# Optimization experiments

Hardware: AMD Instinct MI355X
Metric: run time of the kernel (lower is better)

The kernel has to match this reference:

```python
import jax, jax.numpy as jnp
import numpy as np

NUM_EMBEDDINGS = 1024
EMBEDDING_DIM = 256
COMMITMENT_COST = 0.25


def setup_inputs() -> dict:
    key = jax.random.key(0)
    k1, k2 = jax.random.split(key)
    x = jax.random.normal(k1, (32, EMBEDDING_DIM, 32, 32), dtype=jnp.float32)
    codebook = jax.random.uniform(
        k2, (NUM_EMBEDDINGS, EMBEDDING_DIM), dtype=jnp.float32,
        minval=-1.0 / NUM_EMBEDDINGS, maxval=1.0 / NUM_EMBEDDINGS)
    return {"x": x, "codebook": codebook}


def reference(x, codebook):
    # x: [B, C, H, W] -> [B, H, W, C]
    inputs = jnp.transpose(x, (0, 2, 3, 1))
    B, H, W, D = inputs.shape
    K = codebook.shape[0]
    flat = inputs.reshape(-1, D)  # [N, D]

    # squared L2 distances to each code: [N, K]
    distances = (jnp.sum(flat ** 2, axis=1, keepdims=True)
                 + jnp.sum(codebook ** 2, axis=1)
                 - 2.0 * flat @ codebook.T)
    idx = jnp.argmin(distances, axis=1)  # [N]

    # gather codes (equivalent to one-hot @ codebook, without materializing one-hot)
    quantized = codebook[idx].reshape(inputs.shape)

    e_latent_loss = jnp.mean((jax.lax.stop_gradient(quantized) - inputs) ** 2)
    q_latent_loss = jnp.mean((quantized - jax.lax.stop_gradient(inputs)) ** 2)
    loss = q_latent_loss + COMMITMENT_COST * e_latent_loss

    # straight-through estimator
    quantized_st = inputs + jax.lax.stop_gradient(quantized - inputs)

    # perplexity from code usage histogram (mean of one-hot encodings)
    N = flat.shape[0]
    avg_probs = jnp.zeros((K,), dtype=flat.dtype).at[idx].add(1.0) / N
    perplexity = jnp.exp(-jnp.sum(avg_probs * jnp.log(avg_probs + 1e-10)))

    out = jnp.transpose(quantized_st, (0, 3, 1, 2))  # back to [B, C, H, W]
    return (out, loss, perplexity)
```

## Files before the change

kernel.cpp:

```cpp
#include <hip/hip_runtime.h>
#include <hip/hip_fp16.h>

typedef _Float16 half8 __attribute__((ext_vector_type(8)));
typedef _Float16 half4v __attribute__((ext_vector_type(4)));
typedef __attribute__((ext_vector_type(4))) float f32x4;

#define OUT_ELEMS 8388608


__global__ __launch_bounds__(256) void prep_kernel(const float* __restrict__ cb,
        unsigned short* __restrict__ chs, float* __restrict__ sq,
        int* __restrict__ counts, float* __restrict__ loss) {
    const int t = threadIdx.x;
    if (blockIdx.x == 0) {
        ((int4*)counts)[t] = make_int4(0, 0, 0, 0);
        if (t == 0) *loss = 0.f;
    }
    const int row = blockIdx.x * 16 + (t >> 4);
    const int d0 = (t & 15) * 16;
    const float* src = cb + row * 256 + d0;
    half8 h0, h1;
    float s = 0.f;
#pragma unroll
    for (int i = 0; i < 16; ++i) {
        const float v = src[i];
        s += v * v;
        const _Float16 h = (_Float16)(v * 1024.f);
        if (i < 8) h0[i] = h; else h1[i - 8] = h;
    }
    *(half8*)(chs + row * 256 + d0)     = h0;
    *(half8*)(chs + row * 256 + d0 + 8) = h1;
#pragma unroll
    for (int off = 1; off < 16; off <<= 1) s += __shfl_xor(s, off);
    if ((t & 15) == 0) sq[row] = s;
}

__global__ __launch_bounds__(512, 2) void vq_kernel(
    const float* __restrict__ x, const float* __restrict__ cb,
    const unsigned short* __restrict__ chs, const float* __restrict__ sq,
    int* __restrict__ counts, float* __restrict__ loss_accum,
    float* __restrict__ out)
{
    __shared__ __align__(16) unsigned char Arena[65536];
    __shared__ float mv[4][128];
    __shared__ int   mk[4][128];
    __shared__ float xsqL[128];
    __shared__ int   codeL[128];
    __shared__ float wsum[2];

    const int t = threadIdx.x;
    const int lane = t & 63;
    const int w  = t >> 6;
    const int wg = w >> 1;
    const int wl = w & 1;
    const int m = lane & 15;
    const int q = lane >> 4;
    const int kb = wg << 8;
    const int rowb = wl << 6;
    const int bid = blockIdx.x;
    const int batch = bid >> 3;
    const int hwb = (bid & 7) << 7;

    unsigned short* XL = (unsigned short*)Arena;
    {
        const float* xg = x + (size_t)batch * 262144 + hwb;
#pragma unroll
        for (int p = 0; p < 4; ++p) {
            const int id = p * 512 + t;
            const int c4 = id >> 5;
            const int hw4 = id & 31;
            const float* s0 = xg + (size_t)(c4 * 4) * 1024 + hw4 * 4;
            const f32x4 v0 = *(const f32x4*)(s0);
            const f32x4 v1 = *(const f32x4*)(s0 + 1024);
            const f32x4 v2 = *(const f32x4*)(s0 + 2048);
            const f32x4 v3 = *(const f32x4*)(s0 + 3072);
#pragma unroll
            for (int j = 0; j < 4; ++j) {
                const int hw = hw4 * 4 + j;
                const int e = (((hw & 7) ^ ((hw >> 3) & 7)) << 1);
                half4v hv;
                hv[0] = (_Float16)v0[j];
                hv[1] = (_Float16)v1[j];
                hv[2] = (_Float16)v2[j];
                hv[3] = (_Float16)v3[j];
                *(half4v*)(XL + hw * 256 + ((c4 ^ e) << 2)) = hv;
            }
        }
    }
    __syncthreads();

    half8 Ah[4][8];
#pragma unroll
    for (int f = 0; f < 4; ++f) {
        const int hw = rowb + f * 16 + m;
        const unsigned short* row = XL + hw * 256;
        const int e = (((hw & 7) ^ ((hw >> 3) & 7)) << 1);
        float xs = 0.f;
#pragma unroll
        for (int ks = 0; ks < 8; ++ks) {
            const half8 a = *(const half8*)(row + (((8 * ks + 2 * q) ^ e) << 2));
            Ah[f][ks] = a;
#pragma unroll
            for (int j = 0; j < 8; ++j) { const float fv = (float)a[j]; xs = fmaf(fv, fv, xs); }
        }
        xs += __shfl_xor(xs, 16);
        xs += __shfl_xor(xs, 32);
        if (wg == 0 && q == 0) xsqL[hw] = xs;
    }

    float bestv[4][4];
    int   bestk[4][4];
#pragma unroll
    for (int f = 0; f < 4; ++f)
#pragma unroll
        for (int r = 0; r < 4; ++r) { bestv[f][r] = 3.4e38f; bestk[f][r] = 0; }

    float sc2 = sq[kb + m];

    const unsigned short* bgl = chs + (size_t)(kb + m) * 256 + q * 8;

    for (int s = 0; s < 16; ++s) {
        float sqn = 0.f;
        if (s + 1 < 16) sqn = sq[kb + (s + 1) * 16 + m];
        half8 Bf[8];
        const unsigned short* bp = bgl + s * 4096;
#pragma unroll
        for (int ks = 0; ks < 8; ++ks)
            Bf[ks] = *(const half8*)(bp + ks * 32);
        f32x4 a0 = {0.f,0.f,0.f,0.f}, a1 = {0.f,0.f,0.f,0.f};
        f32x4 a2 = {0.f,0.f,0.f,0.f}, a3 = {0.f,0.f,0.f,0.f};
#pragma unroll
        for (int ks = 0; ks < 8; ++ks) {
            a0 = __builtin_amdgcn_mfma_f32_16x16x32_f16(Ah[0][ks], Bf[ks], a0, 0, 0, 0);
            a1 = __builtin_amdgcn_mfma_f32_16x16x32_f16(Ah[1][ks], Bf[ks], a1, 0, 0, 0);
            a2 = __builtin_amdgcn_mfma_f32_16x16x32_f16(Ah[2][ks], Bf[ks], a2, 0, 0, 0);
            a3 = __builtin_amdgcn_mfma_f32_16x16x32_f16(Ah[3][ks], Bf[ks], a3, 0, 0, 0);
        }
        const int code = kb + s * 16 + m;
#pragma unroll
        for (int f = 0; f < 4; ++f) {
            const f32x4 a = (f == 0) ? a0 : (f == 1) ? a1 : (f == 2) ? a2 : a3;
#pragma unroll
            for (int r = 0; r < 4; ++r) {
                const float d0v = fmaf(-0.001953125f, a[r], sc2);
                if (d0v < bestv[f][r]) { bestv[f][r] = d0v; bestk[f][r] = code; }
            }
        }
        sc2 = sqn;
    }

#pragma unroll
    for (int f = 0; f < 4; ++f)
#pragma unroll
        for (int r = 0; r < 4; ++r) {
            float v = bestv[f][r];
            int   k = bestk[f][r];
#pragma unroll
            for (int d = 1; d < 16; d <<= 1) {
                const float ov = __shfl_xor(v, d);
                const int   ok = __shfl_xor(k, d);
                if (ov < v || (ov == v && ok < k)) { v = ov; k = ok; }
            }
            if (m == 0) {
                const int row = rowb + f * 16 + q * 4 + r;
                mv[wg][row] = v;
                mk[wg][row] = k;
            }
        }
    __syncthreads();

    if (t < 128) {
        float v = mv[0][t]; int k = mk[0][t];
#pragma unroll
        for (int g2 = 1; g2 < 4; ++g2) {
            const float vg = mv[g2][t];
            const int   kg = mk[g2][t];
            if (vg < v) { v = vg; k = kg; }
        }
        codeL[t] = k;
        atomicAdd(&counts[k], 1);
        float lp = xsqL[t] + v;
#pragma unroll
        for (int off = 32; off > 0; off >>= 1) lp += __shfl_down(lp, off);
        if ((t & 63) == 0) wsum[t >> 6] = lp;
    }
    __syncthreads();
    if (t == 0) atomicAdd(loss_accum, wsum[0] + wsum[1]);

    float* Q = (float*)Arena;
#pragma unroll
    for (int h = 0; h < 4; ++h) {
        {
            const int r = t & 31, seg = t >> 5;
            const float* src = cb + (size_t)codeL[h * 32 + r] * 256 + seg * 16;
#pragma unroll
            for (int i = 0; i < 4; ++i)
                *(f32x4*)&Q[r * 257 + seg * 16 + i * 4] = *(const f32x4*)(src + i * 4);
        }
        __syncthreads();
        {
            const int hw4 = (t & 7) * 4;
            const int c0 = t >> 3;
            float* dst = out + (size_t)batch * 262144 + hwb + h * 32 + hw4;
#pragma unroll
            for (int i = 0; i < 4; ++i) {
                const int c = c0 + i * 64;
                f32x4 v;
                v[0] = Q[(hw4 + 0) * 257 + c];
                v[1] = Q[(hw4 + 1) * 257 + c];
                v[2] = Q[(hw4 + 2) * 257 + c];
                v[3] = Q[(hw4 + 3) * 257 + c];
                *(f32x4*)(dst + (size_t)c * 1024) = v;
            }
        }
        if (h < 3) __syncthreads();
    }
}

__global__ __launch_bounds__(256) void finalize_kernel(
    const int* __restrict__ counts, const float* __restrict__ loss_accum,
    float* __restrict__ out)
{
    __shared__ float wsum[4];
    const int t = threadIdx.x;
    float s = 0.f;
#pragma unroll
    for (int mm = 0; mm < 4; ++mm) {
        const float p = (float)counts[t + 256 * mm] * (1.f / 32768.f);
        s += p * logf(p + 1e-10f);
    }
#pragma unroll
    for (int off = 32; off > 0; off >>= 1) s += __shfl_down(s, off);
    if ((t & 63) == 0) wsum[t >> 6] = s;
    __syncthreads();
    if (t == 0) {
        out[OUT_ELEMS]     = loss_accum[0] * (1.25f / 8388608.f);
        out[OUT_ELEMS + 1] = expf(-(wsum[0] + wsum[1] + wsum[2] + wsum[3]));
    }
}

extern "C" void kernel_launch(void* const* d_in, const int* in_sizes, int n_in,
                              void* d_out, int out_size, void* d_ws, size_t ws_size,
                              hipStream_t stream) {
    const float* x  = (const float*)d_in[0];
    const float* cb = (const float*)d_in[1];
    float* out = (float*)d_out;
    char* wsb = (char*)d_ws;
    int*            counts = (int*)(wsb + 0);
    float*          loss   = (float*)(wsb + 4096);
    float*          sq     = (float*)(wsb + 8192);
    unsigned short* chs    = (unsigned short*)(wsb + 16384);

    prep_kernel<<<64, 256, 0, stream>>>(cb, chs, sq, counts, loss);
    vq_kernel<<<256, 512, 0, stream>>>(x, cb, chs, sq, counts, loss, out);
    finalize_kernel<<<1, 256, 0, stream>>>(counts, loss, out);
}
```

Before: 134.7 us.

## Halve rows per block, pre-swizzle codebook fragments, pack best indices, nontemporal IO

```diff
diff --git a/kernel.cpp b/kernel.cpp
--- a/kernel.cpp
+++ b/kernel.cpp
@@ -28,25 +28,28 @@
         const _Float16 h = (_Float16)(v * 1024.f);
         if (i < 8) h0[i] = h; else h1[i - 8] = h;
     }
-    *(half8*)(chs + row * 256 + d0)     = h0;
-    *(half8*)(chs + row * 256 + d0 + 8) = h1;
+    const int g = row >> 8, st = (row >> 4) & 15, m = row & 15;
+    const int j0 = (t & 15) * 2;
+    const int ks = j0 >> 2, qq = j0 & 3;
+    unsigned short* dst = chs + (size_t)((((g * 16 + st) * 8 + ks) * 64) + m * 4 + qq) * 8;
+    *(half8*)dst       = h0;
+    *(half8*)(dst + 8) = h1;
 #pragma unroll
     for (int off = 1; off < 16; off <<= 1) s += __shfl_xor(s, off);
     if ((t & 15) == 0) sq[row] = s;
 }
 
-__global__ __launch_bounds__(512, 2) void vq_kernel(
+__global__ __launch_bounds__(512, 4) void vq_kernel(
     const float* __restrict__ x, const float* __restrict__ cb,
     const unsigned short* __restrict__ chs, const float* __restrict__ sq,
     int* __restrict__ counts, float* __restrict__ loss_accum,
     float* __restrict__ out)
 {
-    __shared__ __align__(16) unsigned char Arena[65536];
-    __shared__ float mv[4][128];
-    __shared__ int   mk[4][128];
-    __shared__ float xsqL[128];
-    __shared__ int   codeL[128];
-    __shared__ float wsum[2];
+    __shared__ __align__(16) unsigned char Arena[33024];
+    __shared__ float mv[4][64];
+    __shared__ int   mk[4][64];
+    __shared__ float xsqL[64];
+    __shared__ int   codeL[64];
 
     const int t = threadIdx.x;
     const int lane = t & 63;
@@ -56,24 +59,24 @@
     const int m = lane & 15;
     const int q = lane >> 4;
     const int kb = wg << 8;
-    const int rowb = wl << 6;
+    const int rowb = wl << 5;
     const int bid = blockIdx.x;
-    const int batch = bid >> 3;
-    const int hwb = (bid & 7) << 7;
+    const int batch = bid >> 4;
+    const int hwb = (bid & 15) << 6;
 
     unsigned short* XL = (unsigned short*)Arena;
     {
         const float* xg = x + (size_t)batch * 262144 + hwb;
 #pragma unroll
-        for (int p = 0; p < 4; ++p) {
+        for (int p = 0; p < 2; ++p) {
             const int id = p * 512 + t;
-            const int c4 = id >> 5;
-            const int hw4 = id & 31;
+            const int c4 = id >> 4;
+            const int hw4 = id & 15;
             const float* s0 = xg + (size_t)(c4 * 4) * 1024 + hw4 * 4;
-            const f32x4 v0 = *(const f32x4*)(s0);
-            const f32x4 v1 = *(const f32x4*)(s0 + 1024);
-            const f32x4 v2 = *(const f32x4*)(s0 + 2048);
-            const f32x4 v3 = *(const f32x4*)(s0 + 3072);
+            const f32x4 v0 = __builtin_nontemporal_load((const f32x4*)(s0));
+            const f32x4 v1 = __builtin_nontemporal_load((const f32x4*)(s0 + 1024));
+            const f32x4 v2 = __builtin_nontemporal_load((const f32x4*)(s0 + 2048));
+            const f32x4 v3 = __builtin_nontemporal_load((const f32x4*)(s0 + 3072));
 #pragma unroll
             for (int j = 0; j < 4; ++j) {
                 const int hw = hw4 * 4 + j;
@@ -89,9 +92,9 @@
     }
     __syncthreads();
 
-    half8 Ah[4][8];
-#pragma unroll
-    for (int f = 0; f < 4; ++f) {
+    half8 Ah[2][8];
+#pragma unroll
+    for (int f = 0; f < 2; ++f) {
         const int hw = rowb + f * 16 + m;
         const unsigned short* row = XL + hw * 256;
         const int e = (((hw & 7) ^ ((hw >> 3) & 7)) << 1);
@@ -108,53 +111,49 @@
         if (wg == 0 && q == 0) xsqL[hw] = xs;
     }
 
-    float bestv[4][4];
-    int   bestk[4][4];
-#pragma unroll
-    for (int f = 0; f < 4; ++f)
-#pragma unroll
-        for (int r = 0; r < 4; ++r) { bestv[f][r] = 3.4e38f; bestk[f][r] = 0; }
-
-    float sc2 = sq[kb + m];
-
-    const unsigned short* bgl = chs + (size_t)(kb + m) * 256 + q * 8;
+    float bestv[2][4];
+#pragma unroll
+    for (int f = 0; f < 2; ++f)
+#pragma unroll
+        for (int r = 0; r < 4; ++r) bestv[f][r] = 3.4e38f;
+    unsigned int bests = 0u;
+
+    const unsigned short* bbase = chs + (size_t)wg * 65536 + (m * 4 + q) * 8;
 
     for (int s = 0; s < 16; ++s) {
-        float sqn = 0.f;
-        if (s + 1 < 16) sqn = sq[kb + (s + 1) * 16 + m];
+        const unsigned short* bp = bbase + s * 4096;
         half8 Bf[8];
-        const unsigned short* bp = bgl + s * 4096;
 #pragma unroll
         for (int ks = 0; ks < 8; ++ks)
-            Bf[ks] = *(const half8*)(bp + ks * 32);
+            Bf[ks] = *(const half8*)(bp + ks * 512);
+        const float sc2 = sq[kb + s * 16 + m];
         f32x4 a0 = {0.f,0.f,0.f,0.f}, a1 = {0.f,0.f,0.f,0.f};
-        f32x4 a2 = {0.f,0.f,0.f,0.f}, a3 = {0.f,0.f,0.f,0.f};
 #pragma unroll
         for (int ks = 0; ks < 8; ++ks) {
             a0 = __builtin_amdgcn_mfma_f32_16x16x32_f16(Ah[0][ks], Bf[ks], a0, 0, 0, 0);
             a1 = __builtin_amdgcn_mfma_f32_16x16x32_f16(Ah[1][ks], Bf[ks], a1, 0, 0, 0);
-            a2 = __builtin_amdgcn_mfma_f32_16x16x32_f16(Ah[2][ks], Bf[ks], a2, 0, 0, 0);
-            a3 = __builtin_amdgcn_mfma_f32_16x16x32_f16(Ah[3][ks], Bf[ks], a3, 0, 0, 0);
-        }
-        const int code = kb + s * 16 + m;
-#pragma unroll
-        for (int f = 0; f < 4; ++f) {
-            const f32x4 a = (f == 0) ? a0 : (f == 1) ? a1 : (f == 2) ? a2 : a3;
+        }
+#pragma unroll
+        for (int f = 0; f < 2; ++f) {
+            const f32x4 a = f ? a1 : a0;
 #pragma unroll
             for (int r = 0; r < 4; ++r) {
                 const float d0v = fmaf(-0.001953125f, a[r], sc2);
-                if (d0v < bestv[f][r]) { bestv[f][r] = d0v; bestk[f][r] = code; }
-            }
-        }
-        sc2 = sqn;
-    }
-
-#pragma unroll
-    for (int f = 0; f < 4; ++f)
+                const int sh = (f * 4 + r) * 4;
+                if (d0v < bestv[f][r]) {
+                    bestv[f][r] = d0v;
+                    bests = (bests & ~(15u << sh)) | ((unsigned)s << sh);
+                }
+            }
+        }
+    }
+
+#pragma unroll
+    for (int f = 0; f < 2; ++f)
 #pragma unroll
         for (int r = 0; r < 4; ++r) {
             float v = bestv[f][r];
-            int   k = bestk[f][r];
+            int   k = kb + (int)((bests >> ((f * 4 + r) * 4)) & 15u) * 16 + m;
 #pragma unroll
             for (int d = 1; d < 16; d <<= 1) {
                 const float ov = __shfl_xor(v, d);
@@ -169,7 +168,7 @@
         }
     __syncthreads();
 
-    if (t < 128) {
+    if (t < 64) {
         float v = mv[0][t]; int k = mk[0][t];
 #pragma unroll
         for (int g2 = 1; g2 < 4; ++g2) {
@@ -182,14 +181,13 @@
         float lp = xsqL[t] + v;
 #pragma unroll
         for (int off = 32; off > 0; off >>= 1) lp += __shfl_down(lp, off);
-        if ((t & 63) == 0) wsum[t >> 6] = lp;
-    }
-    __syncthreads();
-    if (t == 0) atomicAdd(loss_accum, wsum[0] + wsum[1]);
+        if (t == 0) atomicAdd(loss_accum, lp);
+    }
+    __syncthreads();
 
     float* Q = (float*)Arena;
 #pragma unroll
-    for (int h = 0; h < 4; ++h) {
+    for (int h = 0; h < 2; ++h) {
         {
             const int r = t & 31, seg = t >> 5;
             const float* src = cb + (size_t)codeL[h * 32 + r] * 256 + seg * 16;
@@ -210,10 +208,10 @@
                 v[1] = Q[(hw4 + 1) * 257 + c];
                 v[2] = Q[(hw4 + 2) * 257 + c];
                 v[3] = Q[(hw4 + 3) * 257 + c];
-                *(f32x4*)(dst + (size_t)c * 1024) = v;
-            }
-        }
-        if (h < 3) __syncthreads();
+                __builtin_nontemporal_store(v, (f32x4*)(dst + (size_t)c * 1024));
+            }
+        }
+        if (h == 0) __syncthreads();
     }
 }
 
@@ -252,6 +250,6 @@
     unsigned short* chs    = (unsigned short*)(wsb + 16384);
 
     prep_kernel<<<64, 256, 0, stream>>>(cb, chs, sq, counts, loss);
-    vq_kernel<<<256, 512, 0, stream>>>(x, cb, chs, sq, counts, loss, out);
+    vq_kernel<<<512, 512, 0, stream>>>(x, cb, chs, sq, counts, loss, out);
     finalize_kernel<<<1, 256, 0, stream>>>(counts, loss, out);
 }
```

Measured after the change: 127.8 us. 1.05x faster.
